# Kernel optimization log

Hardware: AMD Instinct MI355X
Metric: run time of the kernel (lower is better)

The kernel has to match this reference:

```python
import jax, jax.numpy as jnp
import numpy as np

B, T, F, H, S, E, L = 64, 256, 80, 512, 512, 512, 3


def setup_inputs() -> dict:
    key = jax.random.key(0)
    ks = jax.random.split(key, 16)
    sc = 0.05  # keep LSTM gates in a sane range
    inp = {
        "padded_targets": jax.random.normal(ks[0], (B, T, F), jnp.float32),
        "encoder_out": jax.random.normal(ks[1], (B, S, E), jnp.float32),
        "input_seq_lens": jax.random.randint(ks[2], (B,), S // 2, S + 1, jnp.int32),
        "Wih0": jax.random.normal(ks[3], (4 * H, F + E), jnp.float32) * sc,
        "Whh0": jax.random.normal(ks[4], (4 * H, H), jnp.float32) * sc,
        "b0": jax.random.normal(ks[5], (4 * H,), jnp.float32) * sc,
        "Wih1": jax.random.normal(ks[6], (4 * H, H), jnp.float32) * sc,
        "Whh1": jax.random.normal(ks[7], (4 * H, H), jnp.float32) * sc,
        "b1": jax.random.normal(ks[8], (4 * H,), jnp.float32) * sc,
        "Wih2": jax.random.normal(ks[9], (4 * H, H), jnp.float32) * sc,
        "Whh2": jax.random.normal(ks[10], (4 * H, H), jnp.float32) * sc,
        "b2": jax.random.normal(ks[11], (4 * H,), jnp.float32) * sc,
        "Wq": jax.random.normal(ks[12], (H, E), jnp.float32) * sc,
        "Wfc": jax.random.normal(ks[13], (E, F), jnp.float32) * sc,
        "bfc": jax.random.normal(ks[14], (F,), jnp.float32) * sc,
    }
    return inp


def _lstm_cell(x, h, c, Wih, Whh, b):
    g = x @ Wih.T + h @ Whh.T + b                      # [B, 4H]
    i, f, gg, o = jnp.split(g, 4, axis=-1)             # PyTorch gate order i,f,g,o
    c_new = jax.nn.sigmoid(f) * c + jax.nn.sigmoid(i) * jnp.tanh(gg)
    h_new = jax.nn.sigmoid(o) * jnp.tanh(c_new)
    return h_new, c_new


def _decode(padded_targets, encoder_out, mask_bias, params):
    (Wih0, Whh0, b0, Wih1, Whh1, b1, Wih2, Whh2, b2, Wq, Wfc, bfc) = params
    Wihs = (Wih0, Wih1, Wih2)
    Whhs = (Whh0, Whh1, Whh2)
    bs = (b0, b1, b2)
    scale = 1.0 / jnp.sqrt(jnp.asarray(E, jnp.float32))

    def step(carry, xt):
        hs, cs, ctx = carry                            # hs/cs: tuples of [B,H]; ctx [B,E]
        inp = jnp.concatenate([xt, ctx], axis=1)       # [B, F+E]  (teach=1.0 -> always target)
        new_h, new_c = [], []
        for l in range(L):
            hl, cl = _lstm_cell(inp, hs[l], cs[l], Wihs[l], Whhs[l], bs[l])
            new_h.append(hl)
            new_c.append(cl)
            inp = hl
        q = new_h[-1] @ Wq                             # [B,E]
        scores = jnp.einsum('be,bse->bs', q, encoder_out) * scale + mask_bias
        w = jax.nn.softmax(scores, axis=-1)            # [B,S]
        ctx_new = jnp.einsum('bs,bse->be', w, encoder_out)
        pred = ctx_new @ Wfc + bfc                     # [B,F]
        return (tuple(new_h), tuple(new_c), ctx_new), pred

    h0 = tuple(jnp.zeros((B, H), padded_targets.dtype) for _ in range(L))
    c0 = tuple(jnp.zeros((B, H), padded_targets.dtype) for _ in range(L))
    ctx0 = jnp.zeros((B, E), padded_targets.dtype)
    xs = jnp.swapaxes(padded_targets[:, :-1], 0, 1)    # [T-1, B, F]
    _, preds = jax.lax.scan(step, (h0, c0, ctx0), xs)
    return jnp.swapaxes(preds, 0, 1)                   # [B, T-1, F]


def reference(padded_targets, encoder_out, input_seq_lens,
              Wih0, Whh0, b0, Wih1, Whh1, b1, Wih2, Whh2, b2, Wq, Wfc, bfc):
    valid = jnp.arange(S)[None, :] < input_seq_lens[:, None]     # [B,S]
    mask_bias = jnp.where(valid, 0.0, -1e9).astype(jnp.float32)
    params = (Wih0, Whh0, b0, Wih1, Whh1, b1, Wih2, Whh2, b2, Wq, Wfc, bfc)
    return _decode(padded_targets, encoder_out, mask_bias, params)
```

## Files before the change

### kernel.cpp

```cpp
#include <hip/hip_runtime.h>

#define NBLK 256
#define NTHR 512

typedef float f32x4 __attribute__((ext_vector_type(4)));
typedef unsigned int u32;

__device__ __forceinline__ float sigm(float x){ return 1.f/(1.f+__expf(-x)); }
__device__ __forceinline__ float tanh_(float x){ return 1.f - 2.f/(__expf(2.f*x)+1.f); }

__device__ __forceinline__ float wred_sum(float v){
  #pragma unroll
  for (int off=32; off; off>>=1) v += __shfl_xor(v, off, 64);
  return v;
}

__device__ __forceinline__ u32 cvtpk(float lo, float hi){
  u32 r; asm("v_cvt_pk_bf16_f32 %0,%1,%2":"=v"(r):"v"(lo),"v"(hi)); return r;
}
__device__ __forceinline__ float bflo(u32 u){ return __uint_as_float(u<<16); }
__device__ __forceinline__ float bfhi(u32 u){ return __uint_as_float(u & 0xFFFF0000u); }

__device__ __forceinline__ void st_sysu(u32* p, u32 v){
  __hip_atomic_store(p, v, __ATOMIC_RELAXED, __HIP_MEMORY_SCOPE_AGENT);
}
__device__ __forceinline__ u32 aldu(const u32* p){
  return __hip_atomic_load(p, __ATOMIC_RELAXED, __HIP_MEMORY_SCOPE_AGENT);
}

__device__ __forceinline__ void vmwait0(){
  asm volatile("s_waitcnt vmcnt(0)" ::: "memory");
  __builtin_amdgcn_sched_barrier(0);
}
__device__ __forceinline__ void lgkm0(){
  asm volatile("s_waitcnt lgkmcnt(0)" ::: "memory");
  __builtin_amdgcn_sched_barrier(0);
}

__device__ __forceinline__ void gsync(unsigned* barD, int idx, unsigned& ep){
  ++ep;
  __builtin_amdgcn_s_waitcnt(0);
  __syncthreads();
  if (threadIdx.x == 0){
    const int g = idx >> 4;
    const unsigned epoch = ep;
    bool rootfin = false;
    unsigned o = __hip_atomic_fetch_add(barD + g*32, 1u, __ATOMIC_ACQ_REL, __HIP_MEMORY_SCOPE_AGENT);
    if (o == 15u){
      __hip_atomic_store(barD + g*32, 0u, __ATOMIC_RELAXED, __HIP_MEMORY_SCOPE_AGENT);
      unsigned o2 = __hip_atomic_fetch_add(barD + 8*32, 1u, __ATOMIC_ACQ_REL, __HIP_MEMORY_SCOPE_AGENT);
      if (o2 == 7u){
        __hip_atomic_store(barD + 8*32, 0u, __ATOMIC_RELAXED, __HIP_MEMORY_SCOPE_AGENT);
        __hip_atomic_store(barD + 9*32, epoch, __ATOMIC_RELEASE, __HIP_MEMORY_SCOPE_AGENT);
        rootfin = true;
      }
    }
    if ((idx & 15) == 0){
      if (!rootfin){
        while (__hip_atomic_load(barD + 9*32, __ATOMIC_RELAXED, __HIP_MEMORY_SCOPE_AGENT) < epoch)
          __builtin_amdgcn_s_sleep(1);
      }
      __hip_atomic_store(barD + (10+g)*32, epoch, __ATOMIC_RELEASE, __HIP_MEMORY_SCOPE_AGENT);
    } else {
      while (__hip_atomic_load(barD + (10+g)*32, __ATOMIC_RELAXED, __HIP_MEMORY_SCOPE_AGENT) < epoch)
        __builtin_amdgcn_s_sleep(1);
    }
  }
  __syncthreads();
}

template<bool L0T>
__device__ __forceinline__ void lstm_layer(
    int jt, int bt, int tid,
    const float (&wt)[2][8][2], const float (&wx)[2][4],
    float brA, float brB,
    const u32* __restrict__ inu, float* sc_c,
    u32* __restrict__ dstA, int strA,
    u32* __restrict__ dstB, int strB,
    u32* stage, float* scr, u32* xsu, float* sG4,
    const float* __restrict__ tgt, int t)
{
  const int lane = tid & 63, r = tid >> 6;
  const u32* src = inu + bt*16384;

  if (L0T){
    #pragma unroll
    for (int i=0;i<3;++i){
      const int flat = tid + (i<<9);
      if (flat < 1280){
        const int row = flat/40, col = flat - row*40;
        const float* q = tgt + ((((bt<<5)+row)<<8) + t)*80 + (col<<1);
        xsu[flat] = cvtpk(q[0], q[1]);
      }
    }
  }
  uint4 ld[8];
  #pragma unroll
  for (int i=0;i<8;++i){
    const u32* p = src + (i<<11) + (tid<<2);
    asm volatile("global_load_dwordx4 %0, %1, off sc0 sc1" : "=v"(ld[i]) : "v"(p));
  }
  vmwait0();
  #pragma unroll
  for (int i=0;i<8;++i) *(uint4*)(stage + (i<<11) + (tid<<2)) = ld[i];
  __syncthreads();

  float* sw = scr + r*1024;
  #pragma unroll 1
  for (int ch=0; ch<4; ++ch){
    float pv0[8], pv1[8];
    #pragma unroll
    for (int bb=0; bb<8; ++bb){
      const u32* rowp = stage + ((ch<<3)+bb)*512 + lane;
      float a0=0.f,a1=0.f,a2=0.f,a3=0.f, c0=0.f,c1=0.f,c2=0.f,c3=0.f;
      #pragma unroll
      for (int i=0;i<8;i+=2){
        const u32 e0 = rowp[(i<<6)];
        const u32 e1 = rowp[((i+1)<<6)];
        const float f0=bflo(e0), f1=bfhi(e0), f2=bflo(e1), f3=bfhi(e1);
        a0 = fmaf(wt[0][i][0],   f0, a0);
        a1 = fmaf(wt[0][i][1],   f1, a1);
        a2 = fmaf(wt[0][i+1][0], f2, a2);
        a3 = fmaf(wt[0][i+1][1], f3, a3);
        c0 = fmaf(wt[1][i][0],   f0, c0);
        c1 = fmaf(wt[1][i][1],   f1, c1);
        c2 = fmaf(wt[1][i+1][0], f2, c2);
        c3 = fmaf(wt[1][i+1][1], f3, c3);
      }
      if (L0T && lane < 20){
        const int lrow = (ch<<3)+bb;
        const u32 x0 = xsu[lrow*40 + (lane<<1)];
        const u32 x1 = xsu[lrow*40 + (lane<<1) + 1];
        const float g0=bflo(x0), g1=bfhi(x0), g2=bflo(x1), g3=bfhi(x1);
        a0 = fmaf(wx[0][0], g0, a0); a1 = fmaf(wx[0][1], g1, a1);
        a2 = fmaf(wx[0][2], g2, a2); a3 = fmaf(wx[0][3], g3, a3);
        c0 = fmaf(wx[1][0], g0, c0); c1 = fmaf(wx[1][1], g1, c1);
        c2 = fmaf(wx[1][2], g2, c2); c3 = fmaf(wx[1][3], g3, c3);
      }
      pv0[bb] = (a0+a1)+(a2+a3);
      pv1[bb] = (c0+c1)+(c2+c3);
    }
    #pragma unroll
    for (int bb=0; bb<8; ++bb){
      sw[(bb<<6) + lane]       = pv0[bb];
      sw[512 + (bb<<6) + lane] = pv1[bb];
    }
    lgkm0();
    {
      const int bb2 = lane>>3, m = lane&7;
      const float* pp = sw + (bb2<<6) + (m<<3);
      float v0 = ((pp[0]+pp[1])+(pp[2]+pp[3])) + ((pp[4]+pp[5])+(pp[6]+pp[7]));
      const float* pq = pp + 512;
      float v1 = ((pq[0]+pq[1])+(pq[2]+pq[3])) + ((pq[4]+pq[5])+(pq[6]+pq[7]));
      v0 += __shfl_xor(v0,1,64); v0 += __shfl_xor(v0,2,64); v0 += __shfl_xor(v0,4,64);
      v1 += __shfl_xor(v1,1,64); v1 += __shfl_xor(v1,2,64); v1 += __shfl_xor(v1,4,64);
      if (m==0){
        sG4[(((ch<<3)+bb2)<<4) + r]     = v0 + brA;
        sG4[(((ch<<3)+bb2)<<4) + r + 8] = v1 + brB;
      }
    }
  }
  lgkm0();
  __syncthreads();

  if (tid < 128){
    const int b = tid>>2, jl = tid&3;
    const float* g = sG4 + (b<<4) + (jl<<2);
    const float gi = sigm(g[0]), gf = sigm(g[1]);
    const float gg = tanh_(g[2]), go = sigm(g[3]);
    const float cn = gf*sc_c[tid] + gi*gg;
    sc_c[tid] = cn;
    const float hn = go*tanh_(cn);
    const float hn1 = __shfl(hn, tid^1, 64);
    if (!(tid&1)){
      const u32 hp = cvtpk(hn, hn1);
      const int gb = (bt<<5) + b;
      const int col = (jt<<1) + (jl>>1);
      st_sysu(dstA + gb*strA + col, hp);
      st_sysu(dstB + gb*strB + col, hp);
    }
  }
}

#define ENC_OFF  475648
#define ENC_CNT  8388608
#define WQ_OFF   8864256
#define WQ_CNT   131072

__global__ __launch_bounds__(NTHR, 2)
void sd_kernel(const float* __restrict__ tgt,  const float* __restrict__ enc,
               const int*   __restrict__ lens,
               const float* __restrict__ Wih0, const float* __restrict__ Whh0, const float* __restrict__ b0v,
               const float* __restrict__ Wih1, const float* __restrict__ Whh1, const float* __restrict__ b1v,
               const float* __restrict__ Wih2, const float* __restrict__ Whh2, const float* __restrict__ b2v,
               const float* __restrict__ Wq,   const float* __restrict__ Wfc,  const float* __restrict__ bfc,
               float* __restrict__ out, void* __restrict__ wsv, int ebf)
{
  unsigned* bar = (unsigned*)wsv;
  u32* wsu = (u32*)((char*)wsv + 8192);
  u32* IN0u = wsu;
  u32* IN1u = wsu + 65536;
  u32* IN2u = wsu + 131072;
  u32* H2u  = wsu + 196608;
  u32* encbfu = wsu + ENC_OFF;
  u32* wqbfu  = wsu + WQ_OFF;

  const int w = blockIdx.x, tid = threadIdx.x;
  const int lane = tid & 63, r = tid >> 6;
  const int d = w & 1;
  const int idx = w >> 1;
  const int jt = idx, bt = d;
  unsigned* barD = bar + d*1024;
  unsigned ep = 0;

  __shared__ __attribute__((aligned(16))) u32 SM[26752];
  u32*   stage = SM;
  float* scr   = (float*)(SM + 16384);
  u32*   xsu   = SM + 24576;
  float* sG4   = (float*)(SM + 25856);
  float* sc_c  = (float*)(SM + 26368);
  float* sBig   = (float*)SM;
  float* sVec   = (float*)(SM + 4096);
  float* sSmall = (float*)(SM + 4608);

  const int wrowA = ((r&3)<<9) + (jt<<2) + (r>>2);
  const int wrowB = wrowA + 2;
  float w0r[2][8][2], w1r[2][8][2], w2r[2][8][2], wx0[2][4];
  #pragma unroll
  for (int s=0;s<2;++s){
    const int wr = s ? wrowB : wrowA;
    #pragma unroll
    for (int i=0;i<8;++i){
      const int k = 2*(lane + (i<<6));
      if (k < 512){
        w0r[s][i][0] = Wih0[wr*592 + 80 + k];   w0r[s][i][1] = Wih0[wr*592 + 81 + k];
        w1r[s][i][0] = Wih1[(wr<<9) + k];       w1r[s][i][1] = Wih1[(wr<<9) + k + 1];
        w2r[s][i][0] = Wih2[(wr<<9) + k];       w2r[s][i][1] = Wih2[(wr<<9) + k + 1];
      } else {
        w0r[s][i][0] = Whh0[(wr<<9) + k - 512]; w0r[s][i][1] = Whh0[(wr<<9) + k - 511];
        w1r[s][i][0] = Whh1[(wr<<9) + k - 512]; w1r[s][i][1] = Whh1[(wr<<9) + k - 511];
        w2r[s][i][0] = Whh2[(wr<<9) + k - 512]; w2r[s][i][1] = Whh2[(wr<<9) + k - 511];
      }
    }
    #pragma unroll
    for (int m=0;m<4;++m)
      wx0[s][m] = (lane < 20) ? Wih0[wr*592 + (lane<<2) + m] : 0.f;
  }
  const float br0A=b0v[wrowA], br0B=b0v[wrowB];
  const float br1A=b1v[wrowA], br1B=b1v[wrowB];
  const float br2A=b2v[wrowA], br2B=b2v[wrowB];

  if (tid < 384) sc_c[tid] = 0.f;

  for (int i = idx*NTHR + tid; i < 106496; i += 128*NTHR){
    u32* p;
    if (i < 98304){
      const int buf = i >> 15;
      const int r2  = i & 32767;
      const int par = r2 >> 14;
      const int r3  = r2 & 16383;
      const int b   = (d<<5) + (r3 >> 9);
      const int c   = r3 & 511;
      u32* base = (buf==0) ? IN0u : (buf==1) ? IN1u : IN2u;
      p = base + par*32768 + b*512 + c;
    } else {
      const int r3 = i - 98304;
      const int b  = (d<<5) + (r3 >> 8);
      p = H2u + b*256 + (r3 & 255);
    }
    st_sysu(p, 0u);
  }
  if (ebf){
    for (int i = idx*NTHR + tid; i < 4194304; i += 128*NTHR){
      const int gi = (d<<22) + i;
      st_sysu(encbfu + gi, cvtpk(enc[2*(size_t)gi], enc[2*(size_t)gi+1]));
    }
    u32* wqd = wqbfu + d*131072;
    for (int i = idx*NTHR + tid; i < 131072; i += 128*NTHR){
      const int k = i >> 8, ee = (i & 255) << 1;
      st_sysu(wqd + i, cvtpk(Wq[(k<<9) + ee], Wq[(k<<9) + ee + 1]));
    }
  }
  gsync(barD, idx, ep);

  for (int t=0; t<255; ++t){
    const int p = t & 1, np = p ^ 1;
    u32* IN0p = IN0u + p*32768;  u32* IN0n = IN0u + np*32768;
    u32* IN1p = IN1u + p*32768;  u32* IN1n = IN1u + np*32768;
    u32* IN2p = IN2u + p*32768;  u32* IN2n = IN2u + np*32768;

    lstm_layer<true >(jt,bt,tid, w0r, wx0, br0A, br0B, IN0p, sc_c,
                      IN0n+256, 512, IN1p, 512, stage,scr,xsu,sG4, tgt, t);
    gsync(barD,idx,ep);
    lstm_layer<false>(jt,bt,tid, w1r, wx0, br1A, br1B, IN1p, sc_c+128,
                      IN1n+256, 512, IN2p, 512, stage,scr,xsu,sG4, tgt, t);
    gsync(barD,idx,ep);
    lstm_layer<false>(jt,bt,tid, w2r, wx0, br2A, br2B, IN2p, sc_c+256,
                      IN2n+256, 512, H2u, 256, stage,scr,xsu,sG4, tgt, t);
    gsync(barD,idx,ep);

    {
      const int b_loc = idx & 31, sq = idx >> 5;
      const int b = (d<<5) + b_loc;
      const int len = lens[b];
      if (tid < 256){
        const u32 u = aldu(H2u + b*256 + tid);
        sVec[2*tid]   = bflo(u);
        sVec[2*tid+1] = bfhi(u);
      }
      __syncthreads();
      float qa = 0.f;
      if (ebf){
        const u32* wqb = wqbfu + d*131072 + (tid>>1);
        const u32 sel = tid & 1;
        #pragma unroll 4
        for (int k=0;k<512;++k){
          const u32 u = wqb[k<<8];
          qa = fmaf(sVec[k], sel ? bfhi(u) : bflo(u), qa);
        }
      } else {
        const float* wqp = Wq + tid;
        #pragma unroll 4
        for (int k=0;k<512;++k) qa = fmaf(sVec[k], wqp[(size_t)k<<9], qa);
      }
      __syncthreads();
      sVec[tid] = qa;
      __syncthreads();

      const int wv = tid >> 6;
      const float4 qA = *(const float4*)(sVec + (lane<<3));
      const float4 qB = *(const float4*)(sVec + (lane<<3) + 4);
      float mr = -3.0e38f, lr = 0.f;
      float c0=0,c1=0,c2=0,c3=0,c4=0,c5=0,c6=0,c7=0;
      const float scale = 0.04419417382415922f;
      if (ebf){
        const u32* ebase = encbfu + (((size_t)b)<<17) + (lane<<2);
        #pragma unroll 1
        for (int rr=0; rr<16; ++rr){
          const int srow = (sq<<7) + (wv<<4) + rr;
          if (srow >= len) break;
          const uint4 eu = *(const uint4*)(ebase + ((size_t)srow<<8));
          const float e0=bflo(eu.x), e1=bfhi(eu.x), e2=bflo(eu.y), e3=bfhi(eu.y);
          const float e4=bflo(eu.z), e5=bfhi(eu.z), e6=bflo(eu.w), e7=bfhi(eu.w);
          float d0 = qA.x*e0, d1 = qA.y*e1, d2 = qA.z*e2, d3 = qA.w*e3;
          d0 = fmaf(qB.x, e4, d0); d1 = fmaf(qB.y, e5, d1);
          d2 = fmaf(qB.z, e6, d2); d3 = fmaf(qB.w, e7, d3);
          float dd = wred_sum((d0+d1)+(d2+d3));
          const float sc = dd*scale;
          const float mn = fmaxf(mr, sc);
          const float sf = __expf(mr - mn);
          const float pe = __expf(sc - mn);
          lr = fmaf(lr, sf, pe);
          c0 = fmaf(c0, sf, pe*e0); c1 = fmaf(c1, sf, pe*e1);
          c2 = fmaf(c2, sf, pe*e2); c3 = fmaf(c3, sf, pe*e3);
          c4 = fmaf(c4, sf, pe*e4); c5 = fmaf(c5, sf, pe*e5);
          c6 = fmaf(c6, sf, pe*e6); c7 = fmaf(c7, sf, pe*e7);
          mr = mn;
        }
      } else {
        #pragma unroll 1
        for (int rr=0; rr<16; ++rr){
          const int srow = (sq<<7) + (wv<<4) + rr;
          if (srow >= len) break;
          const float* ep2 = enc + (((size_t)(b<<9)+srow)<<9) + (lane<<3);
          const float4 e0v = *(const float4*)(ep2);
          const float4 e1v = *(const float4*)(ep2+4);
          float d0 = qA.x*e0v.x, d1 = qA.y*e0v.y, d2 = qA.z*e0v.z, d3 = qA.w*e0v.w;
          d0 = fmaf(qB.x, e1v.x, d0); d1 = fmaf(qB.y, e1v.y, d1);
          d2 = fmaf(qB.z, e1v.z, d2); d3 = fmaf(qB.w, e1v.w, d3);
          float dd = wred_sum((d0+d1)+(d2+d3));
          const float sc = dd*scale;
          const float mn = fmaxf(mr, sc);
          const float sf = __expf(mr - mn);
          const float pe = __expf(sc - mn);
          lr = fmaf(lr, sf, pe);
          c0 = fmaf(c0, sf, pe*e0v.x); c1 = fmaf(c1, sf, pe*e0v.y);
          c2 = fmaf(c2, sf, pe*e0v.z); c3 = fmaf(c3, sf, pe*e0v.w);
          c4 = fmaf(c4, sf, pe*e1v.x); c5 = fmaf(c5, sf, pe*e1v.y);
          c6 = fmaf(c6, sf, pe*e1v.z); c7 = fmaf(c7, sf, pe*e1v.w);
          mr = mn;
        }
      }
      if (lane==0){ sSmall[wv] = mr; sSmall[8+wv] = lr; }
      {
        float4 v0 = {c0,c1,c2,c3}, v1 = {c4,c5,c6,c7};
        *(float4*)(sBig + (wv<<9) + (lane<<3))     = v0;
        *(float4*)(sBig + (wv<<9) + (lane<<3) + 4) = v1;
      }
      __syncthreads();
      float M = sSmall[0];
      #pragma unroll
      for (int i=1;i<8;++i) M = fmaxf(M, sSmall[i]);
      float L = 0.f, acc = 0.f;
      #pragma unroll
      for (int i=0;i<8;++i){
        const float A = __expf(sSmall[i]-M);
        L   = fmaf(A, sSmall[8+i], L);
        acc = fmaf(A, sBig[(i<<9)+tid], acc);
      }
      float* PC = (float*)(wsu + 212992);
      float* MS = (float*)(wsu + 212992 + 131072*4/2);
      (void)MS;
      st_sysu((u32*)&PC[(((sq<<6)+b)<<9)+tid], __float_as_uint(acc));
      if (tid==0){
        float* MSS = PC + 131072;
        st_sysu((u32*)&MSS[(((sq<<6)+b)<<1)],   __float_as_uint(M));
        st_sysu((u32*)&MSS[(((sq<<6)+b)<<1)+1], __float_as_uint(L));
      }
    }
    gsync(barD,idx,ep);

    if (idx < 32){
      const int b = (d<<5) + idx;
      float* PC  = (float*)(wsu + 212992);
      float* MSS = PC + 131072;
      const float m0 = __uint_as_float(aldu((u32*)&MSS[(b)<<1]));
      const float S0 = __uint_as_float(aldu((u32*)&MSS[((b)<<1)+1]));
      const float m1 = __uint_as_float(aldu((u32*)&MSS[(64+b)<<1]));
      const float S1 = __uint_as_float(aldu((u32*)&MSS[((64+b)<<1)+1]));
      const float m2 = __uint_as_float(aldu((u32*)&MSS[(128+b)<<1]));
      const float S2 = __uint_as_float(aldu((u32*)&MSS[((128+b)<<1)+1]));
      const float m3 = __uint_as_float(aldu((u32*)&MSS[(192+b)<<1]));
      const float S3 = __uint_as_float(aldu((u32*)&MSS[((192+b)<<1)+1]));
      const float M  = fmaxf(fmaxf(m0,m1), fmaxf(m2,m3));
      const float a0=__expf(m0-M), a1=__expf(m1-M), a2=__expf(m2-M), a3=__expf(m3-M);
      const float inv = 1.f/(a0*S0 + a1*S1 + a2*S2 + a3*S3);
      const float c =
        (a0*__uint_as_float(aldu((u32*)&PC[(b<<9)+tid]))
       + a1*__uint_as_float(aldu((u32*)&PC[((64+b)<<9)+tid]))
       + a2*__uint_as_float(aldu((u32*)&PC[((128+b)<<9)+tid]))
       + a3*__uint_as_float(aldu((u32*)&PC[((192+b)<<9)+tid]))) * inv;
      const float cpr = __shfl(c, tid^1, 64);
      if (!(tid&1)) st_sysu(IN0n + b*512 + (tid>>1), cvtpk(c, cpr));
      sVec[tid] = c;
      __syncthreads();
      if (tid < 80){
        float acc2 = 0.f;
        #pragma unroll 4
        for (int e2=0;e2<512;++e2) acc2 = fmaf(sVec[e2], Wfc[e2*80+tid], acc2);
        out[((size_t)b*255 + t)*80 + tid] = acc2 + bfc[tid];
      }
    }
    gsync(barD,idx,ep);
  }
}

extern "C" void kernel_launch(void* const* d_in, const int* in_sizes, int n_in,
                              void* d_out, int out_size, void* d_ws, size_t ws_size,
                              hipStream_t stream) {
  const float* tgt  = (const float*)d_in[0];
  const float* enc  = (const float*)d_in[1];
  const int*   lens = (const int*)  d_in[2];
  const float* Wih0 = (const float*)d_in[3];
  const float* Whh0 = (const float*)d_in[4];
  const float* b0   = (const float*)d_in[5];
  const float* Wih1 = (const float*)d_in[6];
  const float* Whh1 = (const float*)d_in[7];
  const float* b1   = (const float*)d_in[8];
  const float* Wih2 = (const float*)d_in[9];
  const float* Whh2 = (const float*)d_in[10];
  const float* b2   = (const float*)d_in[11];
  const float* Wq   = (const float*)d_in[12];
  const float* Wfc  = (const float*)d_in[13];
  const float* bfc  = (const float*)d_in[14];

  const size_t need = 8192ull + ((size_t)WQ_OFF + 2ull*(size_t)WQ_CNT)*4ull;
  const int ebf = (ws_size >= need) ? 1 : 0;

  hipMemsetAsync(d_ws, 0, 8192, stream);
  sd_kernel<<<NBLK, NTHR, 0, stream>>>(tgt, enc, lens,
                                       Wih0, Whh0, b0,
                                       Wih1, Whh1, b1,
                                       Wih2, Whh2, b2,
                                       Wq, Wfc, bfc,
                                       (float*)d_out, d_ws, ebf);
}
```

Measured before the change: 31.78 ms.

## Replace hierarchical atomic grid barrier with flag-array gather and broadcast

The grid-wide barrier used to chain atomic fetch-adds through group counters and a root counter, then release group leaders, who in turn released their members. Now each block writes its epoch into its own flag slot. Block 0 polls all 128 slots with one wavefront using a wave-wide vote, then publishes a single release flag that every other block spins on. This cuts the number of serialized hops per barrier and removes atomic read-modify-write contention. In exchange, one block does all the polling, and ordering now relies on relaxed stores placed after a full waitcnt instead of acquire/release atomics.

```diff
diff --git a/kernel.cpp b/kernel.cpp
--- a/kernel.cpp
+++ b/kernel.cpp
@@ -41,29 +41,22 @@
   ++ep;
   __builtin_amdgcn_s_waitcnt(0);
   __syncthreads();
-  if (threadIdx.x == 0){
-    const int g = idx >> 4;
-    const unsigned epoch = ep;
-    bool rootfin = false;
-    unsigned o = __hip_atomic_fetch_add(barD + g*32, 1u, __ATOMIC_ACQ_REL, __HIP_MEMORY_SCOPE_AGENT);
-    if (o == 15u){
-      __hip_atomic_store(barD + g*32, 0u, __ATOMIC_RELAXED, __HIP_MEMORY_SCOPE_AGENT);
-      unsigned o2 = __hip_atomic_fetch_add(barD + 8*32, 1u, __ATOMIC_ACQ_REL, __HIP_MEMORY_SCOPE_AGENT);
-      if (o2 == 7u){
-        __hip_atomic_store(barD + 8*32, 0u, __ATOMIC_RELAXED, __HIP_MEMORY_SCOPE_AGENT);
-        __hip_atomic_store(barD + 9*32, epoch, __ATOMIC_RELEASE, __HIP_MEMORY_SCOPE_AGENT);
-        rootfin = true;
-      }
-    }
-    if ((idx & 15) == 0){
-      if (!rootfin){
-        while (__hip_atomic_load(barD + 9*32, __ATOMIC_RELAXED, __HIP_MEMORY_SCOPE_AGENT) < epoch)
-          __builtin_amdgcn_s_sleep(1);
-      }
-      __hip_atomic_store(barD + (10+g)*32, epoch, __ATOMIC_RELEASE, __HIP_MEMORY_SCOPE_AGENT);
-    } else {
-      while (__hip_atomic_load(barD + (10+g)*32, __ATOMIC_RELAXED, __HIP_MEMORY_SCOPE_AGENT) < epoch)
+  const int tid = threadIdx.x;
+  if (idx == 0){
+    if (tid < 64){
+      if (tid == 0) st_sysu(barD + 256, ep);
+      for (;;){
+        const u32 f0 = aldu(barD + 256 + tid);
+        const u32 f1 = aldu(barD + 320 + tid);
+        if (__all((f0 >= ep) && (f1 >= ep))) break;
         __builtin_amdgcn_s_sleep(1);
+      }
+      if (tid == 0) st_sysu(barD, ep);
+    }
+  } else {
+    if (tid == 0){
+      st_sysu(barD + 256 + idx, ep);
+      while (aldu(barD) < ep) __builtin_amdgcn_s_sleep(1);
     }
   }
   __syncthreads();
@@ -399,8 +392,6 @@
         acc = fmaf(A, sBig[(i<<9)+tid], acc);
       }
       float* PC = (float*)(wsu + 212992);
-      float* MS = (float*)(wsu + 212992 + 131072*4/2);
-      (void)MS;
       st_sysu((u32*)&PC[(((sq<<6)+b)<<9)+tid], __float_as_uint(acc));
       if (tid==0){
         float* MSS = PC + 131072;
```

New measurement: 27.13 ms, median of 2. 1.17x faster.
